# Kernel tuning notes

Hardware: AMD Instinct MI355X
Metric: run time of the kernel (lower is better)

## Reference

```python
import jax, jax.numpy as jnp
import numpy as np

B, T, V, C, D = 32, 512, 25, 64, 128
EPS = 1e-5


def _shift_indices(num_nodes, ch, sign):
    i = np.arange(num_nodes)[:, None]
    j = np.arange(ch)[None, :]
    idx = (i * ch + j + sign * j * ch) % (ch * num_nodes)
    return jnp.asarray(idx.reshape(-1).astype(np.int32))


def setup_inputs() -> dict:
    key = jax.random.key(0)
    ks = jax.random.split(key, 6)
    return {
        "x0": jax.random.normal(ks[0], (B, T, V, C), jnp.float32),
        "feature_mask": jax.random.normal(ks[1], (1, V, C), jnp.float32) * 0.1,
        "W": jax.random.normal(ks[2], (C, D), jnp.float32) * (1.0 / np.sqrt(D)),
        "lin_b": jax.random.normal(ks[3], (1, 1, D), jnp.float32) * 0.02,
        "bn_gamma": jnp.ones((V * D,), jnp.float32),
        "bn_beta": jnp.zeros((V * D,), jnp.float32),
        "down_w": jax.random.normal(ks[4], (D, C), jnp.float32) * (1.0 / np.sqrt(C)),
        "down_b": jax.random.normal(ks[5], (D,), jnp.float32) * 0.02,
        "dbn_gamma": jnp.ones((D,), jnp.float32),
        "dbn_beta": jnp.zeros((D,), jnp.float32),
        "shift_in": _shift_indices(V, C, +1),
        "shift_out": _shift_indices(V, D, -1),
    }


def reference(x0, feature_mask, W, lin_b, bn_gamma, bn_beta,
              down_w, down_b, dbn_gamma, dbn_beta, shift_in, shift_out):
    b, t, v, c = x0.shape
    d = W.shape[1]
    n = b * t
    # shift-in gather over flattened (V*C) feature axis
    x = x0.reshape(n, v * c)[:, shift_in].reshape(n, v, c)
    # learned feature mask
    x = x * (jnp.tanh(feature_mask) + 1.0)
    # small per-node linear
    x = jnp.einsum('nvc,cd->nvd', x, W) + lin_b
    # shift-out gather
    x = x.reshape(n, v * d)[:, shift_out]
    # BatchNorm1d (training-mode batch stats, biased variance)
    mu = x.mean(0)
    var = x.var(0)
    x = (x - mu) * (bn_gamma / jnp.sqrt(var + EPS)) + bn_beta
    x = x.reshape(b, t, v, d).transpose(0, 3, 1, 2)  # (B, D, T, V)
    # residual down path: 1x1 conv == per-position matmul, then BN2d
    res = jnp.einsum('btvc,dc->btvd', x0, down_w) + down_b
    rmu = res.mean((0, 1, 2))
    rvar = res.var((0, 1, 2))
    res = (res - rmu) * (dbn_gamma / jnp.sqrt(rvar + EPS)) + dbn_beta
    res = res.transpose(0, 3, 1, 2)  # (B, D, T, V)
    return jax.nn.relu(x + res)
```

## Files before the change

### kernel.cpp

```cpp
#include <hip/hip_runtime.h>

#define VC 1600
#define EPSF 1e-5f

#define WS_MASKJ  0
#define WS_WPACK  1600
#define WS_DWPACK 5696
#define WS_ABY    9792
#define WS_ABR    16192
#define WS_COLSUM 16448
#define WS_QYP    18048
#define QYP_STRIDE 3328

typedef __attribute__((ext_vector_type(8))) short s16x8;
typedef __attribute__((ext_vector_type(4))) short s16x4;
typedef __attribute__((ext_vector_type(4))) float f32x4;

__device__ __forceinline__ short f2bf(float f) {
  unsigned u = __builtin_bit_cast(unsigned, f);
  u += 0x7fffu + ((u >> 16) & 1u);
  return (short)(u >> 16);
}
__device__ __forceinline__ float bf2f(short s) {
  unsigned u = ((unsigned)(unsigned short)s) << 16;
  return __builtin_bit_cast(float, u);
}

__device__ __forceinline__ void stage_elem(int j, int base, int vstr, float4 xv,
                                           const float* mj, short* s_raw, short* s_xm) {
  int u = j >> 6, c = j & 63;
  s16x4 pk; pk[0]=f2bf(xv.x); pk[1]=f2bf(xv.y); pk[2]=f2bf(xv.z); pk[3]=f2bf(xv.w);
  *(s16x4*)(s_raw + (base + u*vstr)*72 + c) = pk;
  int v0 = (u - c + 75) % 25;
  float xa[4] = {xv.x, xv.y, xv.z, xv.w};
#pragma unroll
  for (int e = 0; e < 4; e++) {
    int ve = v0 - e; if (ve < 0) ve += 25;
    s_xm[(base + ve*vstr)*72 + c + e] = f2bf(xa[e] * mj[e]);
  }
}

__global__ void k_init(const float* __restrict__ fm, const float* __restrict__ W,
                       const float* __restrict__ dw, float* __restrict__ ws) {
  int g = blockIdx.x * 256 + threadIdx.x;
  if (g < VC) {
    int c = g & 63, jv = g >> 6;
    int v = (jv - c + 75) % 25;
    ws[WS_MASKJ + g] = tanhf(fm[v * 64 + c]) + 1.0f;
    ws[WS_COLSUM + g] = 0.0f;
  }
  if (g >= 2048 && g < 3072) {
    int idx = g - 2048;
    int frag = idx >> 6, lane = idx & 63;
    int nt = frag >> 1, k = frag & 1, q = lane >> 4, l = lane & 15;
    s16x8 pk;
#pragma unroll
    for (int j = 0; j < 8; j++) {
      int c = k * 32 + q * 8 + j;
      pk[j] = f2bf(W[c * 128 + nt * 16 + l]);
    }
    ((s16x8*)(ws + WS_WPACK))[idx] = pk;
  }
  if (g >= 3072 && g < 4096) {
    int idx = g - 3072;
    int frag = idx >> 6, lane = idx & 63;
    int nt = frag >> 1, k = frag & 1, q = lane >> 4, l = lane & 15;
    s16x8 pk;
#pragma unroll
    for (int j = 0; j < 8; j++) {
      int c = k * 32 + q * 8 + j;
      pk[j] = f2bf(dw[(nt * 16 + l) * 64 + c]);
    }
    ((s16x8*)(ws + WS_DWPACK))[idx] = pk;
  }
}

__launch_bounds__(256, 2)
__global__ void k_stats(const float* __restrict__ x0, float* __restrict__ ws) {
  __shared__ short s_raw[14976];
  __shared__ short s_xm[14976];
  __shared__ float s_qy[3328];
  int tid = threadIdx.x;
  int wave = tid >> 6, lane = tid & 63, quad = lane >> 4, l15 = lane & 15;
  for (int t = tid; t < 3328; t += 256) s_qy[t] = 0.f;
  for (int t = tid; t < 576; t += 256) { s_raw[14400 + t] = 0; s_xm[14400 + t] = 0; }
  const s16x8* wpack = (const s16x8*)(ws + WS_WPACK);
  const s16x8* dwpack = (const s16x8*)(ws + WS_DWPACK);

  int nt0 = wave * 2;
  s16x8 bw[2][2], bd[2][2];
#pragma unroll
  for (int a = 0; a < 2; a++) {
    int nt = nt0 + a;
    bw[a][0] = wpack[(nt * 2 + 0) * 64 + lane];
    bw[a][1] = wpack[(nt * 2 + 1) * 64 + lane];
    bd[a][0] = dwpack[(nt * 2 + 0) * 64 + lane];
    bd[a][1] = dwpack[(nt * 2 + 1) * 64 + lane];
  }
  float mj0[4], mj1[4];
  {
    float4 m4 = *(const float4*)(ws + WS_MASKJ + tid * 4);
    mj0[0]=m4.x; mj0[1]=m4.y; mj0[2]=m4.z; mj0[3]=m4.w;
  }
  if (tid < 144) {
    float4 m4 = *(const float4*)(ws + WS_MASKJ + 1024 + tid * 4);
    mj1[0]=m4.x; mj1[1]=m4.y; mj1[2]=m4.z; mj1[3]=m4.w;
  }
  float cs[8] = {0,0,0,0,0,0,0,0};
  float rq0 = 0.f, rq1 = 0.f;

  for (int chunk = 0; chunk < 4; chunk++) {
    int n0 = blockIdx.x * 32 + chunk * 8;
    __syncthreads();
    for (int r = 0; r < 8; r++) {
      const float* rowp = x0 + (size_t)(n0 + r) * VC;
      float4 xv = *(const float4*)(rowp + tid * 4);
      cs[0]+=xv.x; cs[1]+=xv.y; cs[2]+=xv.z; cs[3]+=xv.w;
      stage_elem(tid * 4, r, 8, xv, mj0, s_raw, s_xm);
      if (tid < 144) {
        float4 xw = *(const float4*)(rowp + 1024 + tid * 4);
        cs[4]+=xw.x; cs[5]+=xw.y; cs[6]+=xw.z; cs[7]+=xw.w;
        stage_elem(1024 + tid * 4, r, 8, xw, mj1, s_raw, s_xm);
      }
    }
    __syncthreads();
#pragma unroll 1
    for (int vp = 0; vp < 13; vp++) {
      int rb = vp * 16;
      const short* px = s_xm + (rb + l15) * 72 + quad * 8;
      const short* pr = s_raw + (rb + l15) * 72 + quad * 8;
      s16x8 a0 = *(const s16x8*)px;
      s16x8 a1 = *(const s16x8*)(px + 32);
      s16x8 r0 = *(const s16x8*)pr;
      s16x8 r1 = *(const s16x8*)(pr + 32);
      int vq = vp * 2 + (quad >> 1);
#pragma unroll
      for (int a = 0; a < 2; a++) {
        f32x4 acc = {0.f, 0.f, 0.f, 0.f};
        acc = __builtin_amdgcn_mfma_f32_16x16x32_bf16(a0, bw[a][0], acc, 0, 0, 0);
        acc = __builtin_amdgcn_mfma_f32_16x16x32_bf16(a1, bw[a][1], acc, 0, 0, 0);
        float q = acc[0]*acc[0] + acc[1]*acc[1] + acc[2]*acc[2] + acc[3]*acc[3];
        atomicAdd(&s_qy[vq * 128 + (nt0 + a) * 16 + l15], q);
        f32x4 rc = {0.f, 0.f, 0.f, 0.f};
        rc = __builtin_amdgcn_mfma_f32_16x16x32_bf16(r0, bd[a][0], rc, 0, 0, 0);
        rc = __builtin_amdgcn_mfma_f32_16x16x32_bf16(r1, bd[a][1], rc, 0, 0, 0);
        float t2 = rc[0]*rc[0] + rc[1]*rc[1] + rc[2]*rc[2] + rc[3]*rc[3];
        if (a == 0) rq0 += t2; else rq1 += t2;
      }
    }
  }
  __syncthreads();
  atomicAdd(&s_qy[3200 + nt0 * 16 + l15], rq0);
  atomicAdd(&s_qy[3200 + (nt0 + 1) * 16 + l15], rq1);
  __syncthreads();
  float* qp = ws + WS_QYP + (size_t)blockIdx.x * QYP_STRIDE;
  for (int t = tid; t < 3328; t += 256) qp[t] = s_qy[t];
#pragma unroll
  for (int e = 0; e < 4; e++) atomicAdd(ws + WS_COLSUM + tid * 4 + e, cs[e]);
  if (tid < 144) {
#pragma unroll
    for (int e = 0; e < 4; e++) atomicAdd(ws + WS_COLSUM + 1024 + tid * 4 + e, cs[4 + e]);
  }
}

__global__ void k_reduce(const float* __restrict__ gamma, const float* __restrict__ beta,
                         const float* __restrict__ dgamma, const float* __restrict__ dbeta,
                         const float* __restrict__ W, const float* __restrict__ dw,
                         float* __restrict__ ws) {
  int tid = threadIdx.x;
  if (blockIdx.x == 25) {
    __shared__ float s_cs[64];
    if (tid < 64) {
      float s = 0.f;
#pragma unroll
      for (int v = 0; v < 25; v++) s += ws[WS_COLSUM + v * 64 + tid];
      s_cs[tid] = s;
    }
    __syncthreads();
    int d = tid;
    float q = 0.f;
#pragma unroll 8
    for (int b2 = 0; b2 < 512; b2++) q += ws[WS_QYP + (size_t)b2 * QYP_STRIDE + 3200 + d];
    float m = 0.f;
#pragma unroll 8
    for (int c = 0; c < 64; c++) m += s_cs[c] * dw[d * 64 + c];
    m *= (1.0f / 409600.0f);
    float var = q * (1.0f / 409600.0f) - m * m;
    float a = dgamma[d] * rsqrtf(var + EPSF);
    ((float2*)(ws + WS_ABR))[d] = make_float2(a, dbeta[d] - m * a);
    return;
  }
  __shared__ float s_cm[1600];
  for (int t = tid; t < 1600; t += 128)
    s_cm[t] = ws[WS_COLSUM + t] * ws[WS_MASKJ + t];
  __syncthreads();
  int f = blockIdx.x * 128 + tid;
  int v = f >> 7, d = f & 127;
  float q = 0.f;
#pragma unroll 8
  for (int b2 = 0; b2 < 512; b2++) q += ws[WS_QYP + (size_t)b2 * QYP_STRIDE + f];
  float m = 0.f;
  int p = v * 64;
#pragma unroll 8
  for (int c = 0; c < 64; c++) {
    m += s_cm[p] * W[c * 128 + d];
    p += 65; if (p >= VC) p -= VC;
  }
  m *= (1.0f / 16384.0f);
  float var = q * (1.0f / 16384.0f) - m * m;
  int d25 = d % 25;
  int vo = v + d25; if (vo >= 25) vo -= 25;
  int jg = vo * 128 + d;
  float a = gamma[jg] * rsqrtf(var + EPSF);
  ((float2*)(ws + WS_ABY))[f] = make_float2(a, beta[jg] - m * a);
}

__launch_bounds__(256, 2)
__global__ void k_main(const float* __restrict__ x0, const float* __restrict__ ws,
                       float* __restrict__ out) {
  __shared__ short s_raw[112 * 72];
  __shared__ short s_xm[112 * 72];
  __shared__ short s_ybuf[100 * 129];
  int tid = threadIdx.x;
  int wave = tid >> 6, lane = tid & 63, quad = lane >> 4, l15 = lane & 15;
  int n0 = blockIdx.x * 4;
  for (int t = tid; t < 1600; t += 256) {
    int flat = t * 4;
    int nl = flat / VC;
    int j = flat - nl * VC;
    float4 xv = *(const float4*)(x0 + (size_t)n0 * VC + flat);
    float4 m4 = *(const float4*)(ws + WS_MASKJ + j);
    float mj[4] = {m4.x, m4.y, m4.z, m4.w};
    stage_elem(j, nl * 25, 1, xv, mj, s_raw, s_xm);
  }
  __syncthreads();
  const s16x8* wpack = (const s16x8*)(ws + WS_WPACK);
  const float2* aby = (const float2*)(ws + WS_ABY);
  {
    s16x8 b0, b1;
#pragma unroll
    for (int ji = 0; ji < 14; ji++) {
      int job = wave * 14 + ji;
      int nt = job / 7, mt = job - nt * 7;
      if (ji == 0 || ji == 7) {
        b0 = wpack[(nt * 2 + 0) * 64 + lane];
        b1 = wpack[(nt * 2 + 1) * 64 + lane];
      }
      int mbase = mt * 16;
      const short* pa = s_xm + (mbase + l15) * 72 + quad * 8;
      s16x8 a0 = *(const s16x8*)(pa);
      s16x8 a1 = *(const s16x8*)(pa + 32);
      f32x4 acc = {0.f, 0.f, 0.f, 0.f};
      acc = __builtin_amdgcn_mfma_f32_16x16x32_bf16(a0, b0, acc, 0, 0, 0);
      acc = __builtin_amdgcn_mfma_f32_16x16x32_bf16(a1, b1, acc, 0, 0, 0);
      int d = nt * 16 + l15;
      int d25 = d % 25;
#pragma unroll
      for (int i = 0; i < 4; i++) {
        int s = mbase + quad * 4 + i;
        if (s < 100) {
          int r = s / 25;
          int vv = s - r * 25;
          float2 ab = aby[vv * 128 + d];
          float val = acc[i] * ab.x + ab.y;
          int vo = vv + d25; if (vo >= 25) vo -= 25;
          s_ybuf[(r * 25 + vo) * 129 + d] = f2bf(val);
        }
      }
    }
  }
  __syncthreads();
  const s16x8* dwpack = (const s16x8*)(ws + WS_DWPACK);
  const float2* abr = (const float2*)(ws + WS_ABR);
  {
    s16x8 b0, b1; float2 ab = make_float2(0.f, 0.f);
#pragma unroll
    for (int ji = 0; ji < 14; ji++) {
      int job = wave * 14 + ji;
      int nt = job / 7, mt = job - nt * 7;
      if (ji == 0 || ji == 7) {
        b0 = dwpack[(nt * 2 + 0) * 64 + lane];
        b1 = dwpack[(nt * 2 + 1) * 64 + lane];
        ab = abr[nt * 16 + l15];
      }
      int mbase = mt * 16;
      const short* pa = s_raw + (mbase + l15) * 72 + quad * 8;
      s16x8 a0 = *(const s16x8*)(pa);
      s16x8 a1 = *(const s16x8*)(pa + 32);
      f32x4 acc = {0.f, 0.f, 0.f, 0.f};
      acc = __builtin_amdgcn_mfma_f32_16x16x32_bf16(a0, b0, acc, 0, 0, 0);
      acc = __builtin_amdgcn_mfma_f32_16x16x32_bf16(a1, b1, acc, 0, 0, 0);
      int d = nt * 16 + l15;
#pragma unroll
      for (int i = 0; i < 4; i++) {
        int s = mbase + quad * 4 + i;
        if (s < 100) {
          int r = s / 25;
          int vv = s - r * 25;
          int ad = (r * 25 + vv) * 129 + d;
          float val = acc[i] * ab.x + ab.y + bf2f(s_ybuf[ad]);
          val = fmaxf(val, 0.0f);
          s_ybuf[ad] = f2bf(val);
        }
      }
    }
  }
  __syncthreads();
  int b = n0 >> 9, t0 = n0 & 511;
  float* ob = out + (size_t)b * 1638400 + (size_t)t0 * 25;
  for (int it = tid; it < 3200; it += 256) {
    int dd = it / 25;
    int qg = it - dd * 25;
    int q0 = qg * 4;
    float4 o;
    o.x = bf2f(s_ybuf[(q0 + 0) * 129 + dd]);
    o.y = bf2f(s_ybuf[(q0 + 1) * 129 + dd]);
    o.z = bf2f(s_ybuf[(q0 + 2) * 129 + dd]);
    o.w = bf2f(s_ybuf[(q0 + 3) * 129 + dd]);
    *(float4*)(ob + (size_t)dd * 12800 + q0) = o;
  }
}

extern "C" void kernel_launch(void* const* d_in, const int* in_sizes, int n_in,
                              void* d_out, int out_size, void* d_ws, size_t ws_size,
                              hipStream_t stream) {
  const float* x0    = (const float*)d_in[0];
  const float* fm    = (const float*)d_in[1];
  const float* W     = (const float*)d_in[2];
  const float* bn_g  = (const float*)d_in[4];
  const float* bn_b  = (const float*)d_in[5];
  const float* dw    = (const float*)d_in[6];
  const float* dbn_g = (const float*)d_in[8];
  const float* dbn_b = (const float*)d_in[9];
  float* ws = (float*)d_ws;
  float* out = (float*)d_out;
  k_init<<<20, 256, 0, stream>>>(fm, W, dw, ws);
  k_stats<<<512, 256, 0, stream>>>(x0, ws);
  k_reduce<<<26, 128, 0, stream>>>(bn_g, bn_b, dbn_g, dbn_b, W, dw, ws);
  k_main<<<4096, 256, 0, stream>>>(x0, ws, out);
}
```

Measured before the change: 617.4 us.

## Materialize bf16 Y and residual in stats pass; add lightweight output kernel

```diff
diff --git a/kernel.cpp b/kernel.cpp
--- a/kernel.cpp
+++ b/kernel.cpp
@@ -11,6 +11,10 @@
 #define WS_COLSUM 16448
 #define WS_QYP    18048
 #define QYP_STRIDE 3328
+#define WS_ABY2   1721984
+#define WS_Y_SH   3456768
+#define WS_R_SH   55885568
+#define WS_NEED_BYTES 216628736ULL
 
 typedef __attribute__((ext_vector_type(8))) short s16x8;
 typedef __attribute__((ext_vector_type(4))) short s16x4;
@@ -76,7 +80,7 @@
 }
 
 __launch_bounds__(256, 2)
-__global__ void k_stats(const float* __restrict__ x0, float* __restrict__ ws) {
+__global__ void k_stats(const float* __restrict__ x0, float* __restrict__ ws, int do_store) {
   __shared__ short s_raw[14976];
   __shared__ short s_xm[14976];
   __shared__ float s_qy[3328];
@@ -86,6 +90,8 @@
   for (int t = tid; t < 576; t += 256) { s_raw[14400 + t] = 0; s_xm[14400 + t] = 0; }
   const s16x8* wpack = (const s16x8*)(ws + WS_WPACK);
   const s16x8* dwpack = (const s16x8*)(ws + WS_DWPACK);
+  short* wsy = (short*)ws + WS_Y_SH;
+  short* wsr = (short*)ws + WS_R_SH;
 
   int nt0 = wave * 2;
   s16x8 bw[2][2], bd[2][2];
@@ -147,6 +153,27 @@
         float t2 = rc[0]*rc[0] + rc[1]*rc[1] + rc[2]*rc[2] + rc[3]*rc[3];
         if (a == 0) rq0 += t2; else rq1 += t2;
       }
+      if (do_store) {
+        int slot = rb + l15;
+        int vv2 = slot >> 3, rr2 = slot & 7;
+        size_t bsh = (size_t)((n0 + rr2) * 25 + vv2) * 128 + nt0 * 16 + quad * 4;
+#pragma unroll
+        for (int aa = 0; aa < 2; aa++) {
+          f32x4 tY = {0.f, 0.f, 0.f, 0.f};
+          tY = __builtin_amdgcn_mfma_f32_16x16x32_bf16(bw[aa][0], a0, tY, 0, 0, 0);
+          tY = __builtin_amdgcn_mfma_f32_16x16x32_bf16(bw[aa][1], a1, tY, 0, 0, 0);
+          f32x4 tR = {0.f, 0.f, 0.f, 0.f};
+          tR = __builtin_amdgcn_mfma_f32_16x16x32_bf16(bd[aa][0], r0, tR, 0, 0, 0);
+          tR = __builtin_amdgcn_mfma_f32_16x16x32_bf16(bd[aa][1], r1, tR, 0, 0, 0);
+          if (vv2 < 25) {
+            s16x4 ky, kr;
+#pragma unroll
+            for (int e = 0; e < 4; e++) { ky[e] = f2bf(tY[e]); kr[e] = f2bf(tR[e]); }
+            *(s16x4*)(wsy + bsh + aa * 16) = ky;
+            *(s16x4*)(wsr + bsh + aa * 16) = kr;
+          }
+        }
+      }
     }
   }
   __syncthreads();
@@ -166,7 +193,7 @@
 __global__ void k_reduce(const float* __restrict__ gamma, const float* __restrict__ beta,
                          const float* __restrict__ dgamma, const float* __restrict__ dbeta,
                          const float* __restrict__ W, const float* __restrict__ dw,
-                         float* __restrict__ ws) {
+                         float* __restrict__ ws, int do_store) {
   int tid = threadIdx.x;
   if (blockIdx.x == 25) {
     __shared__ float s_cs[64];
@@ -212,7 +239,56 @@
   int vo = v + d25; if (vo >= 25) vo -= 25;
   int jg = vo * 128 + d;
   float a = gamma[jg] * rsqrtf(var + EPSF);
-  ((float2*)(ws + WS_ABY))[f] = make_float2(a, beta[jg] - m * a);
+  float bb = beta[jg] - m * a;
+  ((float2*)(ws + WS_ABY))[f] = make_float2(a, bb);
+  if (do_store) ((float2*)(ws + WS_ABY2))[vo * 128 + d] = make_float2(a, bb);
+}
+
+__launch_bounds__(256, 3)
+__global__ void k_out(const float* __restrict__ ws, float* __restrict__ out) {
+  __shared__ short s_y[12800];
+  __shared__ short s_r[12800];
+  int tid = threadIdx.x;
+  int n0 = blockIdx.x * 4;
+  const short* wsy = (const short*)ws + WS_Y_SH + (size_t)n0 * 3200;
+  const short* wsr = (const short*)ws + WS_R_SH + (size_t)n0 * 3200;
+  for (int idx = tid; idx < 1600; idx += 256) {
+    int tl = idx / 400;
+    int rem = idx - tl * 400;
+    int v = rem >> 4, dblk = rem & 15;
+    int phys = (((tl * 25 + v) << 4) + (dblk ^ (v & 15))) * 8;
+    *(s16x8*)(s_y + phys) = *(const s16x8*)(wsy + idx * 8);
+    *(s16x8*)(s_r + phys) = *(const s16x8*)(wsr + idx * 8);
+  }
+  __syncthreads();
+  int b = n0 >> 9, t0 = n0 & 511;
+  float* ob = out + (size_t)b * 1638400 + (size_t)t0 * 25;
+  const float2* aby2 = (const float2*)(ws + WS_ABY2);
+  const float2* abrp = (const float2*)(ws + WS_ABR);
+  for (int it = tid; it < 3200; it += 256) {
+    int dd = it / 25;
+    int qg = it - dd * 25;
+    int q0 = qg * 4;
+    int d25 = dd % 25;
+    float2 ar = abrp[dd];
+    int tl = q0 / 25;
+    int vo = q0 - tl * 25;
+    int sh = dd >> 3, dlo = dd & 7;
+    float ov[4];
+#pragma unroll
+    for (int e = 0; e < 4; e++) {
+      int vi = vo - d25; if (vi < 0) vi += 25;
+      int ady = (((tl * 25 + vi) << 4) + (sh ^ (vi & 15))) * 8 + dlo;
+      int adr = (((tl * 25 + vo) << 4) + (sh ^ (vo & 15))) * 8 + dlo;
+      float yv = bf2f(s_y[ady]);
+      float rv = bf2f(s_r[adr]);
+      float2 ay = aby2[vo * 128 + dd];
+      ov[e] = fmaxf(yv * ay.x + ay.y + rv * ar.x + ar.y, 0.0f);
+      vo++; if (vo == 25) { vo = 0; tl++; }
+    }
+    float4 o; o.x = ov[0]; o.y = ov[1]; o.z = ov[2]; o.w = ov[3];
+    *(float4*)(ob + (size_t)dd * 12800 + q0) = o;
+  }
 }
 
 __launch_bounds__(256, 2)
@@ -231,7 +307,7 @@
     float4 xv = *(const float4*)(x0 + (size_t)n0 * VC + flat);
     float4 m4 = *(const float4*)(ws + WS_MASKJ + j);
     float mj[4] = {m4.x, m4.y, m4.z, m4.w};
-    stage_elem(j, nl * 25, 1, xv, mj, s_raw, s_xm);
+    stage_elem(j, nl * 25, 1, xv, mj, (short*)s_raw, (short*)s_xm);
   }
   __syncthreads();
   const s16x8* wpack = (const s16x8*)(ws + WS_WPACK);
@@ -334,8 +410,10 @@
   const float* dbn_b = (const float*)d_in[9];
   float* ws = (float*)d_ws;
   float* out = (float*)d_out;
+  int big = (ws_size >= WS_NEED_BYTES) ? 1 : 0;
   k_init<<<20, 256, 0, stream>>>(fm, W, dw, ws);
-  k_stats<<<512, 256, 0, stream>>>(x0, ws);
-  k_reduce<<<26, 128, 0, stream>>>(bn_g, bn_b, dbn_g, dbn_b, W, dw, ws);
-  k_main<<<4096, 256, 0, stream>>>(x0, ws, out);
-}
+  k_stats<<<512, 256, 0, stream>>>(x0, ws, big);
+  k_reduce<<<26, 128, 0, stream>>>(bn_g, bn_b, dbn_g, dbn_b, W, dw, ws, big);
+  if (big) k_out<<<4096, 256, 0, stream>>>(ws, out);
+  else     k_main<<<4096, 256, 0, stream>>>(x0, ws, out);
+}
```

Result: no change. 624.2 us (+1.1%).
